# Kernel tuning notes

Measured on AMD Instinct MI355X. Metric: run time of the kernel, lower is better.

## Reference

```python
import jax, jax.numpy as jnp
import numpy as np

# ---- static config (mirrors GptOssDecoderLayer init) ----
H = 1024      # hidden_size
HD = 64       # head_size
NQ = 16       # num_query_heads
NKV = 4       # num_key_value_heads
G = NQ // NKV # num_key_value_groups
E = 8         # num_experts
TOPK = 2      # experts_per_token
FFN = 1024    # expert intermediate (== hidden in GPT-OSS)
B, Q = 4, 128 # batch sequences, new query tokens per sequence
P, PS = 8, 128
S = P * PS    # kv length per sequence
T = B * Q     # total query tokens
SW = 128      # sliding window (layer_idx % 2 == 0 -> active)
LIMIT = 7.0   # swiglu_limit
ALPHA = 1.702
EPS = 1e-5
NEG = -1e30
SCALE = HD ** -0.5


def rmsnorm(x, w):
    return x * w * jax.lax.rsqrt(jnp.mean(x * x, axis=-1, keepdims=True) + EPS)


def setup_inputs() -> dict:
    key = jax.random.key(0)
    ks = jax.random.split(key, 16)
    hidden = jax.random.normal(ks[0], (T, H), jnp.float32)
    kv_cache = jax.random.normal(ks[1], (B * P, 2, PS, NKV, HD), jnp.float32)
    kv_page_indices = jnp.arange(B * P, dtype=jnp.int32).reshape(B, P)
    # additive causal mask: query q sits at absolute position S - Q + q
    qpos = S - Q + jnp.arange(Q)
    kpos = jnp.arange(S)
    causal = qpos[:, None] >= kpos[None, :]
    attention_mask = jnp.broadcast_to(
        jnp.where(causal, 0.0, NEG).astype(jnp.float32), (B, Q, S))
    sinks = 0.1 * jax.random.normal(ks[2], (NQ,), jnp.float32)
    w_qkv = jax.random.normal(ks[3], (H, HD * (NQ + 2 * NKV)), jnp.float32) / np.sqrt(H)
    b_qkv = jnp.zeros((HD * (NQ + 2 * NKV),), jnp.float32)
    w_o = jax.random.normal(ks[4], (NQ * HD, H), jnp.float32) / np.sqrt(NQ * HD)
    b_o = jnp.zeros((H,), jnp.float32)
    ln1_w = jnp.ones((H,), jnp.float32)
    ln2_w = jnp.ones((H,), jnp.float32)
    w_router = jax.random.normal(ks[5], (H, E), jnp.float32) / np.sqrt(H)
    b_router = jnp.zeros((E,), jnp.float32)
    w_gate_up = jax.random.normal(ks[6], (E, H, 2 * FFN), jnp.float32) / np.sqrt(H)
    b_gate_up = jnp.zeros((E, 2 * FFN), jnp.float32)
    w_down = jax.random.normal(ks[7], (E, FFN, H), jnp.float32) / np.sqrt(FFN)
    b_down = jnp.zeros((E, H), jnp.float32)
    return dict(hidden=hidden, kv_cache=kv_cache, attention_mask=attention_mask,
                kv_page_indices=kv_page_indices, sinks=sinks, w_qkv=w_qkv,
                b_qkv=b_qkv, w_o=w_o, b_o=b_o, ln1_w=ln1_w, ln2_w=ln2_w,
                w_router=w_router, b_router=b_router, w_gate_up=w_gate_up,
                b_gate_up=b_gate_up, w_down=w_down, b_down=b_down)


def reference(hidden, kv_cache, attention_mask, kv_page_indices, sinks,
              w_qkv, b_qkv, w_o, b_o, ln1_w, ln2_w, w_router, b_router,
              w_gate_up, b_gate_up, w_down, b_down):
    # ---- attention block ----
    x = rmsnorm(hidden, ln1_w)
    qkv = x @ w_qkv + b_qkv                       # [T, HD*(NQ+2*NKV)]
    q = qkv[:, :NQ * HD].reshape(B, Q, NQ, HD)
    k_new = qkv[:, NQ * HD:(NQ + NKV) * HD].reshape(B, Q, NKV, HD)
    v_new = qkv[:, (NQ + NKV) * HD:].reshape(B, Q, NKV, HD)
    # gather paged KV cache -> [B, S, NKV, HD]; write new tokens into tail slots
    pages = kv_cache[kv_page_indices]             # [B, P, 2, PS, NKV, HD]
    K = pages[:, :, 0].reshape(B, S, NKV, HD).at[:, S - Q:].set(k_new)
    V = pages[:, :, 1].reshape(B, S, NKV, HD).at[:, S - Q:].set(v_new)
    Kr = jnp.repeat(K, G, axis=2)                 # GQA expand -> [B, S, NQ, HD]
    Vr = jnp.repeat(V, G, axis=2)
    scores = jnp.einsum('bqhd,bshd->bhqs', q * SCALE, Kr) + attention_mask[:, None]
    # sliding-window (module trims pages outside the window; equivalent mask)
    qpos = S - Q + jnp.arange(Q)
    kpos = jnp.arange(S)
    win_ok = (qpos[:, None] - kpos[None, :]) < SW
    scores = jnp.where(win_ok[None, None], scores, NEG)
    m = jnp.max(scores, axis=-1)
    m = jnp.where(jnp.isinf(m) & (m < 0), 0.0, m)
    p = jnp.exp(scores - m[..., None])            # [B, NQ, Q, S]
    # attention sink joins the softmax denominator (online-softmax correction)
    denom = jnp.sum(p, axis=-1) + jnp.exp(sinks[None, :, None] - m)
    attn = jnp.einsum('bhqs,bshd->bhqd', p, Vr) / denom[..., None]
    attn = attn.transpose(0, 2, 1, 3).reshape(T, NQ * HD)
    h = hidden + attn @ w_o + b_o
    # ---- MoE block ----
    x2 = rmsnorm(h, ln2_w)
    logits = x2 @ w_router + b_router             # [T, E]
    vals, idx = jax.lax.top_k(logits, TOPK)
    wts = jax.nn.softmax(vals, axis=-1)
    comb = jnp.sum(jax.nn.one_hot(idx, E, dtype=x2.dtype) * wts[..., None], axis=1)
    gu = jnp.einsum('th,ehf->etf', x2, w_gate_up) + b_gate_up[:, None, :]
    gate = jnp.minimum(gu[..., 0::2], LIMIT)
    up = jnp.clip(gu[..., 1::2], -LIMIT, LIMIT)
    glu = gate * jax.nn.sigmoid(gate * ALPHA)
    eo = jnp.einsum('etf,efh->eth', (up + 1.0) * glu, w_down) + b_down[:, None, :]
    moe = jnp.einsum('te,eth->th', comb, eo)
    return h + moe
```

## Files before the change

### kernel.cpp

```cpp
#include <hip/hip_runtime.h>

constexpr int H    = 1024;
constexpr int HD   = 64;
constexpr int NQ   = 16;
constexpr int NKV  = 4;
constexpr int E_   = 8;
constexpr int FFN  = 1024;
constexpr int B_   = 4;
constexpr int Q_   = 128;
constexpr int P_   = 8;
constexpr int PS   = 128;
constexpr int S_   = P_ * PS;
constexpr int T_   = B_ * Q_;
constexpr int QKV_N = HD * (NQ + 2 * NKV);
constexpr float EPS   = 1e-5f;
constexpr float ALPHA = 1.702f;
constexpr float LIMIT = 7.0f;
constexpr float SCALE = 0.125f;

constexpr int MAXROWS = 1536;
constexpr int MAXTILES = 24;

typedef __attribute__((ext_vector_type(4))) float f32x4;
typedef __attribute__((ext_vector_type(8))) short s16x8;

__device__ __forceinline__ unsigned short f2bf(float f) {
    unsigned u = __float_as_uint(f);
    u += 0x7FFFu + ((u >> 16) & 1u);
    return (unsigned short)(u >> 16);
}

__device__ __forceinline__ void lds_barrier() {
    asm volatile("s_waitcnt lgkmcnt(0)" ::: "memory");
    __builtin_amdgcn_s_barrier();
}

__global__ __launch_bounds__(256) void rmsnorm_kernel(const float* __restrict__ in,
                                                      const float* __restrict__ w,
                                                      unsigned short* __restrict__ outb,
                                                      int* __restrict__ cnt) {
    int t   = blockIdx.x;
    int tid = threadIdx.x;
    if (t == 0 && tid < E_) cnt[tid] = 0;
    float4 v = ((const float4*)(in + (size_t)t * H))[tid];
    float ss = v.x * v.x + v.y * v.y + v.z * v.z + v.w * v.w;
#pragma unroll
    for (int off = 32; off; off >>= 1) ss += __shfl_down(ss, off);
    __shared__ float partial[4];
    __shared__ float s_inv;
    if ((tid & 63) == 0) partial[tid >> 6] = ss;
    __syncthreads();
    if (tid == 0)
        s_inv = rsqrtf((partial[0] + partial[1] + partial[2] + partial[3]) * (1.0f / H) + EPS);
    __syncthreads();
    float inv = s_inv;
    float4 wv = ((const float4*)w)[tid];
    ushort4 ob;
    ob.x = f2bf(v.x * wv.x * inv); ob.y = f2bf(v.y * wv.y * inv);
    ob.z = f2bf(v.z * wv.z * inv); ob.w = f2bf(v.w * wv.w * inv);
    ((ushort4*)(outb + (size_t)t * H))[tid] = ob;
}

__global__ __launch_bounds__(256) void gemm_dense_t(const unsigned short* __restrict__ Abf,
                                                    const float* __restrict__ W,
                                                    const float* __restrict__ bias,
                                                    const float* __restrict__ resid,
                                                    float* __restrict__ C,
                                                    float* __restrict__ Cdup, int N) {
    int nb = blockIdx.x, mb = blockIdx.y * 64;
    int tid = threadIdx.x;
    int w = tid >> 6, lane = tid & 63;
    int r16 = lane & 15, kq = lane >> 4;
    int skb = tid >> 5, sn = tid & 31;

    __shared__ unsigned short WtA[8][32][8];
    __shared__ unsigned short WtB[8][32][8];

    size_t sN = (size_t)N;
    const float* wsrc = W + (size_t)(skb * 8) * sN + nb * 32 + sn;
    const unsigned short* ap = Abf + (size_t)(mb + w * 16 + r16) * 1024 + kq * 8;

    float wrA[8], wrB[8];
    s16x8 afA0, afA1, afB0, afB1;
    f32x4 acc0 = {}, acc1 = {};

#pragma unroll
    for (int j = 0; j < 8; j++) wrA[j] = wsrc[(size_t)j * sN];
    {
        s16x8 p;
#pragma unroll
        for (int j = 0; j < 8; j++) p[j] = (short)f2bf(wrA[j]);
        *(s16x8*)&WtA[skb][sn][0] = p;
    }
#pragma unroll
    for (int j = 0; j < 8; j++) wrA[j] = wsrc[(size_t)(64 + j) * sN];
    afA0 = *(const s16x8*)(ap);
    afA1 = *(const s16x8*)(ap + 32);
    lds_barrier();

    for (int s = 0; s < 8; s++) {
        int t0 = 2 * s;
        s16x8 b00 = *(const s16x8*)&WtA[kq][r16][0];
        s16x8 b01 = *(const s16x8*)&WtA[kq][16 + r16][0];
        s16x8 b10 = *(const s16x8*)&WtA[4 + kq][r16][0];
        s16x8 b11 = *(const s16x8*)&WtA[4 + kq][16 + r16][0];
        afB0 = *(const s16x8*)(ap + (t0 + 1) * 64);
        afB1 = *(const s16x8*)(ap + (t0 + 1) * 64 + 32);
        if (s < 7) {
#pragma unroll
            for (int j = 0; j < 8; j++) wrB[j] = wsrc[(size_t)((t0 + 2) * 64 + j) * sN];
        }
        acc0 = __builtin_amdgcn_mfma_f32_16x16x32_bf16(afA0, b00, acc0, 0, 0, 0);
        acc1 = __builtin_amdgcn_mfma_f32_16x16x32_bf16(afA0, b01, acc1, 0, 0, 0);
        acc0 = __builtin_amdgcn_mfma_f32_16x16x32_bf16(afA1, b10, acc0, 0, 0, 0);
        acc1 = __builtin_amdgcn_mfma_f32_16x16x32_bf16(afA1, b11, acc1, 0, 0, 0);
        {
            s16x8 p;
#pragma unroll
            for (int j = 0; j < 8; j++) p[j] = (short)f2bf(wrA[j]);
            *(s16x8*)&WtB[skb][sn][0] = p;
        }
        lds_barrier();
        s16x8 c00 = *(const s16x8*)&WtB[kq][r16][0];
        s16x8 c01 = *(const s16x8*)&WtB[kq][16 + r16][0];
        s16x8 c10 = *(const s16x8*)&WtB[4 + kq][r16][0];
        s16x8 c11 = *(const s16x8*)&WtB[4 + kq][16 + r16][0];
        if (s < 7) {
            afA0 = *(const s16x8*)(ap + (t0 + 2) * 64);
            afA1 = *(const s16x8*)(ap + (t0 + 2) * 64 + 32);
#pragma unroll
            for (int j = 0; j < 8; j++) wrA[j] = wsrc[(size_t)((t0 + 3) * 64 + j) * sN];
        }
        acc0 = __builtin_amdgcn_mfma_f32_16x16x32_bf16(afB0, c00, acc0, 0, 0, 0);
        acc1 = __builtin_amdgcn_mfma_f32_16x16x32_bf16(afB0, c01, acc1, 0, 0, 0);
        acc0 = __builtin_amdgcn_mfma_f32_16x16x32_bf16(afB1, c10, acc0, 0, 0, 0);
        acc1 = __builtin_amdgcn_mfma_f32_16x16x32_bf16(afB1, c11, acc1, 0, 0, 0);
        if (s < 7) {
            s16x8 p;
#pragma unroll
            for (int j = 0; j < 8; j++) p[j] = (short)f2bf(wrB[j]);
            *(s16x8*)&WtA[skb][sn][0] = p;
        }
        lds_barrier();
    }

    int row0 = mb + w * 16 + kq * 4;
    f32x4 accs[2] = {acc0, acc1};
#pragma unroll
    for (int nf = 0; nf < 2; nf++) {
        int col = nb * 32 + nf * 16 + r16;
        float bcol = bias[col];
#pragma unroll
        for (int r = 0; r < 4; r++) {
            int row = row0 + r;
            float v = accs[nf][r] + bcol;
            if (resid) v += resid[(size_t)row * sN + col];
            C[(size_t)row * sN + col] = v;
            if (Cdup) Cdup[(size_t)row * sN + col] = v;
        }
    }
}

__global__ __launch_bounds__(256) void attn_group_kernel(const float* __restrict__ qkv,
                                                         const float* __restrict__ kv_cache,
                                                         const int* __restrict__ page_idx,
                                                         const float* __restrict__ sinks,
                                                         unsigned short* __restrict__ attn_bf) {
    int blk = blockIdx.x;
    int kvh = blk & 3;
    int q   = (blk >> 2) & 127;
    int b   = blk >> 9;
    int t   = b * Q_ + q;
    int tid = threadIdx.x;
    int s_lo = S_ - Q_ - 127 + q;

    __shared__ __align__(16) float Vs[128][64];
    __shared__ __align__(16) float qs4[4][64];
    __shared__ float pv[4][128];
    __shared__ float sD[4];

#pragma unroll
    for (int r = 0; r < 8; r++) {
        int l = r * 256 + tid;
        int key = l >> 4, c = l & 15;
        int s = s_lo + key;
        const float* vp;
        if (s < S_ - Q_) {
            int page = page_idx[b * P_ + (s >> 7)];
            vp = kv_cache + (size_t)page * 65536 + 32768 + (size_t)(s & 127) * (NKV * HD) + kvh * HD;
        } else {
            vp = qkv + (size_t)(b * Q_ + (s - (S_ - Q_))) * QKV_N + (NQ + NKV) * HD + kvh * HD;
        }
        ((float4*)Vs[key])[c] = *(const float4*)(vp + c * 4);
    }
    {
        int hh = tid >> 6, d2 = tid & 63;
        qs4[hh][d2] = qkv[(size_t)t * QKV_N + (kvh * 4 + hh) * HD + d2];
    }
    __syncthreads();

    {
        int key = tid & 127, hp = tid >> 7;
        int s = s_lo + key;
        const float* kp;
        if (s < S_ - Q_) {
            int page = page_idx[b * P_ + (s >> 7)];
            kp = kv_cache + (size_t)page * 65536 + (size_t)(s & 127) * (NKV * HD) + kvh * HD;
        } else {
            kp = qkv + (size_t)(b * Q_ + (s - (S_ - Q_))) * QKV_N + NQ * HD + kvh * HD;
        }
        const float4* kp4 = (const float4*)kp;
        const float4* q0p = (const float4*)qs4[hp * 2];
        const float4* q1p = (const float4*)qs4[hp * 2 + 1];
        float sc0 = 0.f, sc1 = 0.f;
#pragma unroll
        for (int d4 = 0; d4 < 16; d4++) {
            float4 kk = kp4[d4];
            float4 q0 = q0p[d4], q1 = q1p[d4];
            sc0 += q0.x * kk.x + q0.y * kk.y + q0.z * kk.z + q0.w * kk.w;
            sc1 += q1.x * kk.x + q1.y * kk.y + q1.z * kk.z + q1.w * kk.w;
        }
        pv[hp * 2][key]     = sc0 * SCALE;
        pv[hp * 2 + 1][key] = sc1 * SCALE;
    }
    __syncthreads();

    {
        int wv = tid >> 6, lane = tid & 63;
        float a0 = pv[wv][lane], a1 = pv[wv][lane + 64];
        float m = fmaxf(a0, a1);
#pragma unroll
        for (int off = 32; off; off >>= 1) m = fmaxf(m, __shfl_xor(m, off));
        float p0 = __expf(a0 - m), p1 = __expf(a1 - m);
        float l = p0 + p1;
#pragma unroll
        for (int off = 32; off; off >>= 1) l += __shfl_xor(l, off);
        pv[wv][lane] = p0;
        pv[wv][lane + 64] = p1;
        if (lane == 0) sD[wv] = l + __expf(sinks[kvh * 4 + wv] - m);
    }
    __syncthreads();

    {
        int hh = tid >> 6, d2 = tid & 63;
        float a0 = 0.f, a1 = 0.f, a2 = 0.f, a3 = 0.f;
#pragma unroll 4
        for (int i = 0; i < 128; i += 4) {
            a0 += pv[hh][i]     * Vs[i][d2];
            a1 += pv[hh][i + 1] * Vs[i + 1][d2];
            a2 += pv[hh][i + 2] * Vs[i + 2][d2];
            a3 += pv[hh][i + 3] * Vs[i + 3][d2];
        }
        float acc = ((a0 + a1) + (a2 + a3)) / sD[hh];
        attn_bf[(size_t)t * (NQ * HD) + (kvh * 4 + hh) * HD + d2] = f2bf(acc);
    }
}

__global__ __launch_bounds__(256) void rms_router_kernel(const float* __restrict__ hbuf,
                                                         const float* __restrict__ ln2w,
                                                         const float* __restrict__ w_router,
                                                         const float* __restrict__ b_router,
                                                         unsigned short* __restrict__ x2bf,
                                                         int* __restrict__ ridx,
                                                         float* __restrict__ rwt,
                                                         int* __restrict__ cnt) {
    int t = blockIdx.x;
    int tid = threadIdx.x;
    float4 v = ((const float4*)(hbuf + (size_t)t * H))[tid];
    float ss = v.x * v.x + v.y * v.y + v.z * v.z + v.w * v.w;
#pragma unroll
    for (int off = 32; off; off >>= 1) ss += __shfl_down(ss, off);
    __shared__ float partial[4];
    __shared__ float s_inv;
    if ((tid & 63) == 0) partial[tid >> 6] = ss;
    __syncthreads();
    if (tid == 0)
        s_inv = rsqrtf((partial[0] + partial[1] + partial[2] + partial[3]) * (1.0f / H) + EPS);
    __syncthreads();
    float inv = s_inv;
    float4 wv = ((const float4*)ln2w)[tid];
    float4 o;
    o.x = v.x * wv.x * inv; o.y = v.y * wv.y * inv;
    o.z = v.z * wv.z * inv; o.w = v.w * wv.w * inv;
    ushort4 ob;
    ob.x = f2bf(o.x); ob.y = f2bf(o.y); ob.z = f2bf(o.z); ob.w = f2bf(o.w);
    ((ushort4*)(x2bf + (size_t)t * H))[tid] = ob;

    const float4* wr = (const float4*)(w_router + (size_t)tid * 4 * E_);
    float p[E_];
    {
        float4 r0a = wr[0], r0b = wr[1];
        float4 r1a = wr[2], r1b = wr[3];
        float4 r2a = wr[4], r2b = wr[5];
        float4 r3a = wr[6], r3b = wr[7];
        p[0] = o.x * r0a.x + o.y * r1a.x + o.z * r2a.x + o.w * r3a.x;
        p[1] = o.x * r0a.y + o.y * r1a.y + o.z * r2a.y + o.w * r3a.y;
        p[2] = o.x * r0a.z + o.y * r1a.z + o.z * r2a.z + o.w * r3a.z;
        p[3] = o.x * r0a.w + o.y * r1a.w + o.z * r2a.w + o.w * r3a.w;
        p[4] = o.x * r0b.x + o.y * r1b.x + o.z * r2b.x + o.w * r3b.x;
        p[5] = o.x * r0b.y + o.y * r1b.y + o.z * r2b.y + o.w * r3b.y;
        p[6] = o.x * r0b.z + o.y * r1b.z + o.z * r2b.z + o.w * r3b.z;
        p[7] = o.x * r0b.w + o.y * r1b.w + o.z * r2b.w + o.w * r3b.w;
    }
    __shared__ float wsum[4][E_];
    int wv2 = tid >> 6, lane = tid & 63;
#pragma unroll
    for (int e = 0; e < E_; e++) {
        float r = p[e];
#pragma unroll
        for (int off = 32; off; off >>= 1) r += __shfl_xor(r, off);
        if (lane == 0) wsum[wv2][e] = r;
    }
    __syncthreads();
    __shared__ float logits[E_];
    if (tid < E_)
        logits[tid] = wsum[0][tid] + wsum[1][tid] + wsum[2][tid] + wsum[3][tid] + b_router[tid];
    __syncthreads();
    if (tid == 0) {
        int i0 = 0; float v0 = logits[0];
        for (int ee = 1; ee < E_; ee++)
            if (logits[ee] > v0) { v0 = logits[ee]; i0 = ee; }
        int i1 = -1; float v1 = -3.4e38f;
        for (int ee = 0; ee < E_; ee++)
            if (ee != i0 && logits[ee] > v1) { v1 = logits[ee]; i1 = ee; }
        float w0 = 1.0f / (1.0f + __expf(v1 - v0));
        ridx[t * 2] = i0; ridx[t * 2 + 1] = i1;
        rwt[t * 2] = w0;  rwt[t * 2 + 1] = 1.0f - w0;
        atomicAdd(&cnt[i0], 1);
        atomicAdd(&cnt[i1], 1);
    }
}

__global__ __launch_bounds__(256) void plumb_kernel(const int* __restrict__ cnt,
                                                    const int* __restrict__ ridx,
                                                    int* __restrict__ poff,
                                                    int* __restrict__ list,
                                                    int* __restrict__ tmap) {
    __shared__ int lpos[E_], lpoff[E_];
    int tid = threadIdx.x;
    if (tid == 0) {
        int run = 0, it = 0;
        for (int e = 0; e < E_; e++) {
            lpoff[e] = run; poff[e] = run;
            int pc = (cnt[e] + 63) & ~63;
            for (int tl = 0; tl < (pc >> 6); tl++) tmap[1 + it++] = (e << 5) | tl;
            run += pc;
        }
        tmap[0] = it;
    }
    if (tid < E_) lpos[tid] = 0;
    __syncthreads();
    for (int i = tid; i < 2 * T_; i += 256) {
        int e = ridx[i];
        int pp = atomicAdd(&lpos[e], 1);
        list[lpoff[e] + pp] = i;
    }
}

__global__ __launch_bounds__(256) void moe_gateup_t(const unsigned short* __restrict__ x2bf,
                                                    const int* __restrict__ list,
                                                    const int* __restrict__ cnt,
                                                    const int* __restrict__ poff,
                                                    const int* __restrict__ tmap,
                                                    const float* __restrict__ wgu,
                                                    const float* __restrict__ bgu,
                                                    unsigned short* __restrict__ act_bf) {
    if ((int)blockIdx.y >= tmap[0]) return;
    int v0m = tmap[1 + blockIdx.y];
    int e = v0m >> 5, tl = v0m & 31;
    int n = cnt[e];
    int base = poff[e];
    int nb = blockIdx.x;
    int tid = threadIdx.x;
    int w = tid >> 6, lane = tid & 63;
    int r16 = lane & 15, kq = lane >> 4;
    int skb = tid >> 5, sn = tid & 31;

    __shared__ unsigned short WtA[8][32][8];
    __shared__ unsigned short WtB[8][32][8];

    const float* wsrc = wgu + (size_t)e * (1024 * 2048) + (size_t)(skb * 8) * 2048 + nb * 32 + sn;
    int rr0 = tl * 64 + w * 16 + r16;
    int t2a = (rr0 < n) ? list[base + rr0] : list[base];
    const unsigned short* ap = x2bf + (size_t)(t2a >> 1) * 1024 + kq * 8;

    float wrA[8], wrB[8];
    s16x8 afA0, afA1, afB0, afB1;
    f32x4 acc0 = {}, acc1 = {};

#pragma unroll
    for (int j = 0; j < 8; j++) wrA[j] = wsrc[(size_t)j * 2048];
    {
        s16x8 p;
#pragma unroll
        for (int j = 0; j < 8; j++) p[j] = (short)f2bf(wrA[j]);
        *(s16x8*)&WtA[skb][sn][0] = p;
    }
#pragma unroll
    for (int j = 0; j < 8; j++) wrA[j] = wsrc[(size_t)(64 + j) * 2048];
    afA0 = *(const s16x8*)(ap);
    afA1 = *(const s16x8*)(ap + 32);
    lds_barrier();

    for (int s = 0; s < 8; s++) {
        int t0 = 2 * s;
        s16x8 b00 = *(const s16x8*)&WtA[kq][r16][0];
        s16x8 b01 = *(const s16x8*)&WtA[kq][16 + r16][0];
        s16x8 b10 = *(const s16x8*)&WtA[4 + kq][r16][0];
        s16x8 b11 = *(const s16x8*)&WtA[4 + kq][16 + r16][0];
        afB0 = *(const s16x8*)(ap + (t0 + 1) * 64);
        afB1 = *(const s16x8*)(ap + (t0 + 1) * 64 + 32);
        if (s < 7) {
#pragma unroll
            for (int j = 0; j < 8; j++) wrB[j] = wsrc[(size_t)((t0 + 2) * 64 + j) * 2048];
        }
        acc0 = __builtin_amdgcn_mfma_f32_16x16x32_bf16(afA0, b00, acc0, 0, 0, 0);
        acc1 = __builtin_amdgcn_mfma_f32_16x16x32_bf16(afA0, b01, acc1, 0, 0, 0);
        acc0 = __builtin_amdgcn_mfma_f32_16x16x32_bf16(afA1, b10, acc0, 0, 0, 0);
        acc1 = __builtin_amdgcn_mfma_f32_16x16x32_bf16(afA1, b11, acc1, 0, 0, 0);
        {
            s16x8 p;
#pragma unroll
            for (int j = 0; j < 8; j++) p[j] = (short)f2bf(wrA[j]);
            *(s16x8*)&WtB[skb][sn][0] = p;
        }
        lds_barrier();
        s16x8 c00 = *(const s16x8*)&WtB[kq][r16][0];
        s16x8 c01 = *(const s16x8*)&WtB[kq][16 + r16][0];
        s16x8 c10 = *(const s16x8*)&WtB[4 + kq][r16][0];
        s16x8 c11 = *(const s16x8*)&WtB[4 + kq][16 + r16][0];
        if (s < 7) {
            afA0 = *(const s16x8*)(ap + (t0 + 2) * 64);
            afA1 = *(const s16x8*)(ap + (t0 + 2) * 64 + 32);
#pragma unroll
            for (int j = 0; j < 8; j++) wrA[j] = wsrc[(size_t)((t0 + 3) * 64 + j) * 2048];
        }
        acc0 = __builtin_amdgcn_mfma_f32_16x16x32_bf16(afB0, c00, acc0, 0, 0, 0);
        acc1 = __builtin_amdgcn_mfma_f32_16x16x32_bf16(afB0, c01, acc1, 0, 0, 0);
        acc0 = __builtin_amdgcn_mfma_f32_16x16x32_bf16(afB1, c10, acc0, 0, 0, 0);
        acc1 = __builtin_amdgcn_mfma_f32_16x16x32_bf16(afB1, c11, acc1, 0, 0, 0);
        if (s < 7) {
            s16x8 p;
#pragma unroll
            for (int j = 0; j < 8; j++) p[j] = (short)f2bf(wrB[j]);
            *(s16x8*)&WtA[skb][sn][0] = p;
        }
        lds_barrier();
    }

    int parity = r16 & 1;
    f32x4 accs[2] = {acc0, acc1};
#pragma unroll
    for (int nf = 0; nf < 2; nf++) {
        int gucol = nb * 32 + nf * 16 + r16;
        float bb = bgu[(size_t)e * 2048 + gucol];
#pragma unroll
        for (int r = 0; r < 4; r++) {
            float v = accs[nf][r] + bb;
            float o = __shfl_xor(v, 1);
            if (!parity) {
                float g = fminf(v, LIMIT);
                float u = fminf(fmaxf(o, -LIMIT), LIMIT);
                float glu = g / (1.0f + __expf(-ALPHA * g));
                int rr = tl * 64 + w * 16 + kq * 4 + r;
                if (rr < n)
                    act_bf[(size_t)(base + rr) * FFN + (gucol >> 1)] = f2bf((u + 1.0f) * glu);
            }
        }
    }
}

__global__ __launch_bounds__(256) void moe_down_t(const unsigned short* __restrict__ act_bf,
                                                  const int* __restrict__ list,
                                                  const int* __restrict__ cnt,
                                                  const int* __restrict__ poff,
                                                  const int* __restrict__ tmap,
                                                  const float* __restrict__ rwt,
                                                  const float* __restrict__ wdn,
                                                  const float* __restrict__ b_down,
                                                  float* __restrict__ out) {
    if ((int)blockIdx.y >= tmap[0]) return;
    int v0m = tmap[1 + blockIdx.y];
    int e = v0m >> 5, tl = v0m & 31;
    int n = cnt[e];
    int base = poff[e];
    int nb = blockIdx.x;
    int z  = blockIdx.z;
    int tid = threadIdx.x;
    int w = tid >> 6, lane = tid & 63;
    int r16 = lane & 15, kq = lane >> 4;
    int skb = tid >> 5, sn = tid & 31;

    __shared__ unsigned short WtA[8][32][8];
    __shared__ unsigned short WtB[8][32][8];

    const float* wsrc = wdn + (size_t)e * (1024 * 1024) + (size_t)(z * 512 + skb * 8) * 1024 + nb * 32 + sn;
    const unsigned short* ap = act_bf + (size_t)(base + tl * 64 + w * 16 + r16) * 1024 + z * 512 + kq * 8;

    float wrA[8], wrB[8];
    s16x8 afA0, afA1, afB0, afB1;
    f32x4 acc0 = {}, acc1 = {};

#pragma unroll
    for (int j = 0; j < 8; j++) wrA[j] = wsrc[(size_t)j * 1024];
    {
        s16x8 p;
#pragma unroll
        for (int j = 0; j < 8; j++) p[j] = (short)f2bf(wrA[j]);
        *(s16x8*)&WtA[skb][sn][0] = p;
    }
#pragma unroll
    for (int j = 0; j < 8; j++) wrA[j] = wsrc[(size_t)(64 + j) * 1024];
    afA0 = *(const s16x8*)(ap);
    afA1 = *(const s16x8*)(ap + 32);
    lds_barrier();

    for (int s = 0; s < 4; s++) {
        int t0 = 2 * s;
        s16x8 b00 = *(const s16x8*)&WtA[kq][r16][0];
        s16x8 b01 = *(const s16x8*)&WtA[kq][16 + r16][0];
        s16x8 b10 = *(const s16x8*)&WtA[4 + kq][r16][0];
        s16x8 b11 = *(const s16x8*)&WtA[4 + kq][16 + r16][0];
        afB0 = *(const s16x8*)(ap + (t0 + 1) * 64);
        afB1 = *(const s16x8*)(ap + (t0 + 1) * 64 + 32);
        if (s < 3) {
#pragma unroll
            for (int j = 0; j < 8; j++) wrB[j] = wsrc[(size_t)((t0 + 2) * 64 + j) * 1024];
        }
        acc0 = __builtin_amdgcn_mfma_f32_16x16x32_bf16(afA0, b00, acc0, 0, 0, 0);
        acc1 = __builtin_amdgcn_mfma_f32_16x16x32_bf16(afA0, b01, acc1, 0, 0, 0);
        acc0 = __builtin_amdgcn_mfma_f32_16x16x32_bf16(afA1, b10, acc0, 0, 0, 0);
        acc1 = __builtin_amdgcn_mfma_f32_16x16x32_bf16(afA1, b11, acc1, 0, 0, 0);
        {
            s16x8 p;
#pragma unroll
            for (int j = 0; j < 8; j++) p[j] = (short)f2bf(wrA[j]);
            *(s16x8*)&WtB[skb][sn][0] = p;
        }
        lds_barrier();
        s16x8 c00 = *(const s16x8*)&WtB[kq][r16][0];
        s16x8 c01 = *(const s16x8*)&WtB[kq][16 + r16][0];
        s16x8 c10 = *(const s16x8*)&WtB[4 + kq][r16][0];
        s16x8 c11 = *(const s16x8*)&WtB[4 + kq][16 + r16][0];
        if (s < 3) {
            afA0 = *(const s16x8*)(ap + (t0 + 2) * 64);
            afA1 = *(const s16x8*)(ap + (t0 + 2) * 64 + 32);
#pragma unroll
            for (int j = 0; j < 8; j++) wrA[j] = wsrc[(size_t)((t0 + 3) * 64 + j) * 1024];
        }
        acc0 = __builtin_amdgcn_mfma_f32_16x16x32_bf16(afB0, c00, acc0, 0, 0, 0);
        acc1 = __builtin_amdgcn_mfma_f32_16x16x32_bf16(afB0, c01, acc1, 0, 0, 0);
        acc0 = __builtin_amdgcn_mfma_f32_16x16x32_bf16(afB1, c10, acc0, 0, 0, 0);
        acc1 = __builtin_amdgcn_mfma_f32_16x16x32_bf16(afB1, c11, acc1, 0, 0, 0);
        if (s < 3) {
            s16x8 p;
#pragma unroll
            for (int j = 0; j < 8; j++) p[j] = (short)f2bf(wrB[j]);
            *(s16x8*)&WtA[skb][sn][0] = p;
        }
        lds_barrier();
    }

    f32x4 accs[2] = {acc0, acc1};
#pragma unroll
    for (int r = 0; r < 4; r++) {
        int rr = tl * 64 + w * 16 + kq * 4 + r;
        if (rr < n) {
            int t2 = list[base + rr];
            float sc = rwt[t2];
            float* op = out + (size_t)(t2 >> 1) * H;
#pragma unroll
            for (int nf = 0; nf < 2; nf++) {
                int col = nb * 32 + nf * 16 + r16;
                float v = accs[nf][r] + (z == 0 ? b_down[(size_t)e * 1024 + col] : 0.0f);
                atomicAdd(op + col, sc * v);
            }
        }
    }
}

extern "C" void kernel_launch(void* const* d_in, const int* in_sizes, int n_in,
                              void* d_out, int out_size, void* d_ws, size_t ws_size,
                              hipStream_t stream) {
    const float* hidden          = (const float*)d_in[0];
    const float* kv_cache        = (const float*)d_in[1];
    const int*   kv_page_indices = (const int*)d_in[3];
    const float* sinks           = (const float*)d_in[4];
    const float* w_qkv           = (const float*)d_in[5];
    const float* b_qkv           = (const float*)d_in[6];
    const float* w_o             = (const float*)d_in[7];
    const float* b_o             = (const float*)d_in[8];
    const float* ln1_w           = (const float*)d_in[9];
    const float* ln2_w           = (const float*)d_in[10];
    const float* w_router        = (const float*)d_in[11];
    const float* b_router        = (const float*)d_in[12];
    const float* w_gate_up       = (const float*)d_in[13];
    const float* b_gate_up       = (const float*)d_in[14];
    const float* w_down          = (const float*)d_in[15];
    const float* b_down          = (const float*)d_in[16];
    float* out = (float*)d_out;

    char* base = (char*)d_ws;
    float* qkv   = (float*)base;                       base += (size_t)T_ * QKV_N * 4;
    float* hbuf  = (float*)base;                       base += (size_t)T_ * H * 4;
    unsigned short* x_bf    = (unsigned short*)base;   base += (size_t)T_ * H * 2;
    unsigned short* x2_bf   = (unsigned short*)base;   base += (size_t)T_ * H * 2;
    unsigned short* attn_bf = (unsigned short*)base;   base += (size_t)T_ * NQ * HD * 2;
    unsigned short* act_bf  = (unsigned short*)base;   base += (size_t)(MAXROWS + 128) * FFN * 2;
    float* rwt  = (float*)base;                        base += 2 * T_ * 4;
    int*   ridx = (int*)base;                          base += 2 * T_ * 4;
    int*   cnt  = (int*)base;                          base += E_ * 4;
    int*   poff = (int*)base;                          base += E_ * 4;
    int*   list = (int*)base;                          base += MAXROWS * 4;
    int*   tmap = (int*)base;                          base += (1 + MAXTILES + 7) * 4;

    rmsnorm_kernel<<<T_, 256, 0, stream>>>(hidden, ln1_w, x_bf, cnt);
    gemm_dense_t<<<dim3(QKV_N / 32, T_ / 64), 256, 0, stream>>>(
        x_bf, w_qkv, b_qkv, nullptr, qkv, nullptr, QKV_N);
    attn_group_kernel<<<B_ * Q_ * NKV, 256, 0, stream>>>(qkv, kv_cache, kv_page_indices, sinks, attn_bf);
    gemm_dense_t<<<dim3(H / 32, T_ / 64), 256, 0, stream>>>(
        attn_bf, w_o, b_o, hidden, hbuf, out, H);
    rms_router_kernel<<<T_, 256, 0, stream>>>(hbuf, ln2_w, w_router, b_router,
                                              x2_bf, ridx, rwt, cnt);
    plumb_kernel<<<1, 256, 0, stream>>>(cnt, ridx, poff, list, tmap);
    moe_gateup_t<<<dim3(FFN * 2 / 32, MAXTILES), 256, 0, stream>>>(
        x2_bf, list, cnt, poff, tmap, w_gate_up, b_gate_up, act_bf);
    moe_down_t<<<dim3(H / 32, MAXTILES, 2), 256, 0, stream>>>(
        act_bf, list, cnt, poff, tmap, rwt, w_down, b_down, out);
}
```

Measured before the change: 275.3 us.

## Split-K the dense GEMMs in two with atomic accumulation and pre-initialized outputs

Adds an init kernel that pre-fills the qkv buffer with its bias and hbuf/out with hidden plus the output bias. Both dense GEMMs are then launched with a z dimension of 2, each half covering 512 of the K range, and their partial sums are accumulated with float atomicAdd. This doubles the block count to fill more compute units for these small-N GEMMs. In exchange it costs an extra launch, memory traffic for the init pass, atomic write contention, and run-to-run nondeterministic summation order.

```diff
diff --git a/kernel.cpp b/kernel.cpp
--- a/kernel.cpp
+++ b/kernel.cpp
@@ -35,6 +35,30 @@
     __builtin_amdgcn_s_barrier();
 }
 
+__global__ __launch_bounds__(256) void init_outputs(const float* __restrict__ hidden,
+                                                    const float* __restrict__ b_qkv,
+                                                    const float* __restrict__ b_o,
+                                                    float* __restrict__ qkv,
+                                                    float* __restrict__ hbuf,
+                                                    float* __restrict__ out) {
+    int i = blockIdx.x * 256 + threadIdx.x;
+    constexpr int NQKV4 = T_ * QKV_N / 4;
+    constexpr int NH4   = T_ * H / 4;
+    if (i < NQKV4) {
+        ((float4*)qkv)[i] = ((const float4*)b_qkv)[i % (QKV_N / 4)];
+    } else {
+        int j = i - NQKV4;
+        if (j < NH4) {
+            float4 h = ((const float4*)hidden)[j];
+            float4 b = ((const float4*)b_o)[j % (H / 4)];
+            float4 v;
+            v.x = h.x + b.x; v.y = h.y + b.y; v.z = h.z + b.z; v.w = h.w + b.w;
+            ((float4*)hbuf)[j] = v;
+            ((float4*)out)[j] = v;
+        }
+    }
+}
+
 __global__ __launch_bounds__(256) void rmsnorm_kernel(const float* __restrict__ in,
                                                       const float* __restrict__ w,
                                                       unsigned short* __restrict__ outb,
@@ -63,11 +87,10 @@
 
 __global__ __launch_bounds__(256) void gemm_dense_t(const unsigned short* __restrict__ Abf,
                                                     const float* __restrict__ W,
-                                                    const float* __restrict__ bias,
-                                                    const float* __restrict__ resid,
                                                     float* __restrict__ C,
                                                     float* __restrict__ Cdup, int N) {
     int nb = blockIdx.x, mb = blockIdx.y * 64;
+    int z  = blockIdx.z;
     int tid = threadIdx.x;
     int w = tid >> 6, lane = tid & 63;
     int r16 = lane & 15, kq = lane >> 4;
@@ -77,8 +100,8 @@
     __shared__ unsigned short WtB[8][32][8];
 
     size_t sN = (size_t)N;
-    const float* wsrc = W + (size_t)(skb * 8) * sN + nb * 32 + sn;
-    const unsigned short* ap = Abf + (size_t)(mb + w * 16 + r16) * 1024 + kq * 8;
+    const float* wsrc = W + (size_t)(z * 512 + skb * 8) * sN + nb * 32 + sn;
+    const unsigned short* ap = Abf + (size_t)(mb + w * 16 + r16) * 1024 + z * 512 + kq * 8;
 
     float wrA[8], wrB[8];
     s16x8 afA0, afA1, afB0, afB1;
@@ -98,7 +121,7 @@
     afA1 = *(const s16x8*)(ap + 32);
     lds_barrier();
 
-    for (int s = 0; s < 8; s++) {
+    for (int s = 0; s < 4; s++) {
         int t0 = 2 * s;
         s16x8 b00 = *(const s16x8*)&WtA[kq][r16][0];
         s16x8 b01 = *(const s16x8*)&WtA[kq][16 + r16][0];
@@ -106,7 +129,7 @@
         s16x8 b11 = *(const s16x8*)&WtA[4 + kq][16 + r16][0];
         afB0 = *(const s16x8*)(ap + (t0 + 1) * 64);
         afB1 = *(const s16x8*)(ap + (t0 + 1) * 64 + 32);
-        if (s < 7) {
+        if (s < 3) {
 #pragma unroll
             for (int j = 0; j < 8; j++) wrB[j] = wsrc[(size_t)((t0 + 2) * 64 + j) * sN];
         }
@@ -125,7 +148,7 @@
         s16x8 c01 = *(const s16x8*)&WtB[kq][16 + r16][0];
         s16x8 c10 = *(const s16x8*)&WtB[4 + kq][r16][0];
         s16x8 c11 = *(const s16x8*)&WtB[4 + kq][16 + r16][0];
-        if (s < 7) {
+        if (s < 3) {
             afA0 = *(const s16x8*)(ap + (t0 + 2) * 64);
             afA1 = *(const s16x8*)(ap + (t0 + 2) * 64 + 32);
 #pragma unroll
@@ -135,7 +158,7 @@
         acc1 = __builtin_amdgcn_mfma_f32_16x16x32_bf16(afB0, c01, acc1, 0, 0, 0);
         acc0 = __builtin_amdgcn_mfma_f32_16x16x32_bf16(afB1, c10, acc0, 0, 0, 0);
         acc1 = __builtin_amdgcn_mfma_f32_16x16x32_bf16(afB1, c11, acc1, 0, 0, 0);
-        if (s < 7) {
+        if (s < 3) {
             s16x8 p;
 #pragma unroll
             for (int j = 0; j < 8; j++) p[j] = (short)f2bf(wrB[j]);
@@ -149,14 +172,11 @@
 #pragma unroll
     for (int nf = 0; nf < 2; nf++) {
         int col = nb * 32 + nf * 16 + r16;
-        float bcol = bias[col];
 #pragma unroll
         for (int r = 0; r < 4; r++) {
             int row = row0 + r;
-            float v = accs[nf][r] + bcol;
-            if (resid) v += resid[(size_t)row * sN + col];
-            C[(size_t)row * sN + col] = v;
-            if (Cdup) Cdup[(size_t)row * sN + col] = v;
+            atomicAdd(&C[(size_t)row * sN + col], accs[nf][r]);
+            if (Cdup) atomicAdd(&Cdup[(size_t)row * sN + col], accs[nf][r]);
         }
     }
 }
@@ -614,12 +634,14 @@
     int*   list = (int*)base;                          base += MAXROWS * 4;
     int*   tmap = (int*)base;                          base += (1 + MAXTILES + 7) * 4;
 
+    init_outputs<<<(T_ * QKV_N / 4 + T_ * H / 4 + 255) / 256, 256, 0, stream>>>(
+        hidden, b_qkv, b_o, qkv, hbuf, out);
     rmsnorm_kernel<<<T_, 256, 0, stream>>>(hidden, ln1_w, x_bf, cnt);
-    gemm_dense_t<<<dim3(QKV_N / 32, T_ / 64), 256, 0, stream>>>(
-        x_bf, w_qkv, b_qkv, nullptr, qkv, nullptr, QKV_N);
+    gemm_dense_t<<<dim3(QKV_N / 32, T_ / 64, 2), 256, 0, stream>>>(
+        x_bf, w_qkv, qkv, nullptr, QKV_N);
     attn_group_kernel<<<B_ * Q_ * NKV, 256, 0, stream>>>(qkv, kv_cache, kv_page_indices, sinks, attn_bf);
-    gemm_dense_t<<<dim3(H / 32, T_ / 64), 256, 0, stream>>>(
-        attn_bf, w_o, b_o, hidden, hbuf, out, H);
+    gemm_dense_t<<<dim3(H / 32, T_ / 64, 2), 256, 0, stream>>>(
+        attn_bf, w_o, hbuf, out, H);
     rms_router_kernel<<<T_, 256, 0, stream>>>(hbuf, ln2_w, w_router, b_router,
                                               x2_bf, ridx, rwt, cnt);
     plumb_kernel<<<1, 256, 0, stream>>>(cnt, ridx, poff, list, tmap);
```

Result: slower. 281.7 us (+2.3%).

## Split-K the MoE gate-up GEMM and move SwiGLU into a separate reduction kernel

Applied to the files above, without the earlier changes.

Splits the gate-up expert GEMM along K into two halves on a third grid dimension, doubling the block count. Each half writes raw fp32 partial sums to a new workspace buffer. A new swiglu kernel sums the two partials, adds the bias, applies the clamped SwiGLU and writes bf16 activations. The aim is better GPU occupancy on the weight-bandwidth-bound GEMM, at the cost of an extra launch and extra fp32 global traffic for the partials.

```diff
diff --git a/kernel.cpp b/kernel.cpp
--- a/kernel.cpp
+++ b/kernel.cpp
@@ -357,20 +357,20 @@
     }
 }
 
-__global__ __launch_bounds__(256) void moe_gateup_t(const unsigned short* __restrict__ x2bf,
-                                                    const int* __restrict__ list,
-                                                    const int* __restrict__ cnt,
-                                                    const int* __restrict__ poff,
-                                                    const int* __restrict__ tmap,
-                                                    const float* __restrict__ wgu,
-                                                    const float* __restrict__ bgu,
-                                                    unsigned short* __restrict__ act_bf) {
+__global__ __launch_bounds__(256) void moe_gateup_sk(const unsigned short* __restrict__ x2bf,
+                                                     const int* __restrict__ list,
+                                                     const int* __restrict__ cnt,
+                                                     const int* __restrict__ poff,
+                                                     const int* __restrict__ tmap,
+                                                     const float* __restrict__ wgu,
+                                                     float* __restrict__ gupart) {
     if ((int)blockIdx.y >= tmap[0]) return;
     int v0m = tmap[1 + blockIdx.y];
     int e = v0m >> 5, tl = v0m & 31;
     int n = cnt[e];
     int base = poff[e];
     int nb = blockIdx.x;
+    int z  = blockIdx.z;
     int tid = threadIdx.x;
     int w = tid >> 6, lane = tid & 63;
     int r16 = lane & 15, kq = lane >> 4;
@@ -379,10 +379,10 @@
     __shared__ unsigned short WtA[8][32][8];
     __shared__ unsigned short WtB[8][32][8];
 
-    const float* wsrc = wgu + (size_t)e * (1024 * 2048) + (size_t)(skb * 8) * 2048 + nb * 32 + sn;
+    const float* wsrc = wgu + (size_t)e * (1024 * 2048) + (size_t)(z * 512 + skb * 8) * 2048 + nb * 32 + sn;
     int rr0 = tl * 64 + w * 16 + r16;
     int t2a = (rr0 < n) ? list[base + rr0] : list[base];
-    const unsigned short* ap = x2bf + (size_t)(t2a >> 1) * 1024 + kq * 8;
+    const unsigned short* ap = x2bf + (size_t)(t2a >> 1) * 1024 + z * 512 + kq * 8;
 
     float wrA[8], wrB[8];
     s16x8 afA0, afA1, afB0, afB1;
@@ -402,7 +402,7 @@
     afA1 = *(const s16x8*)(ap + 32);
     lds_barrier();
 
-    for (int s = 0; s < 8; s++) {
+    for (int s = 0; s < 4; s++) {
         int t0 = 2 * s;
         s16x8 b00 = *(const s16x8*)&WtA[kq][r16][0];
         s16x8 b01 = *(const s16x8*)&WtA[kq][16 + r16][0];
@@ -410,7 +410,7 @@
         s16x8 b11 = *(const s16x8*)&WtA[4 + kq][16 + r16][0];
         afB0 = *(const s16x8*)(ap + (t0 + 1) * 64);
         afB1 = *(const s16x8*)(ap + (t0 + 1) * 64 + 32);
-        if (s < 7) {
+        if (s < 3) {
 #pragma unroll
             for (int j = 0; j < 8; j++) wrB[j] = wsrc[(size_t)((t0 + 2) * 64 + j) * 2048];
         }
@@ -429,7 +429,7 @@
         s16x8 c01 = *(const s16x8*)&WtB[kq][16 + r16][0];
         s16x8 c10 = *(const s16x8*)&WtB[4 + kq][r16][0];
         s16x8 c11 = *(const s16x8*)&WtB[4 + kq][16 + r16][0];
-        if (s < 7) {
+        if (s < 3) {
             afA0 = *(const s16x8*)(ap + (t0 + 2) * 64);
             afA1 = *(const s16x8*)(ap + (t0 + 2) * 64 + 32);
 #pragma unroll
@@ -439,7 +439,7 @@
         acc1 = __builtin_amdgcn_mfma_f32_16x16x32_bf16(afB0, c01, acc1, 0, 0, 0);
         acc0 = __builtin_amdgcn_mfma_f32_16x16x32_bf16(afB1, c10, acc0, 0, 0, 0);
         acc1 = __builtin_amdgcn_mfma_f32_16x16x32_bf16(afB1, c11, acc1, 0, 0, 0);
-        if (s < 7) {
+        if (s < 3) {
             s16x8 p;
 #pragma unroll
             for (int j = 0; j < 8; j++) p[j] = (short)f2bf(wrB[j]);
@@ -448,25 +448,45 @@
         lds_barrier();
     }
 
-    int parity = r16 & 1;
+    float* gp = gupart + (size_t)z * MAXROWS * 2048;
     f32x4 accs[2] = {acc0, acc1};
 #pragma unroll
     for (int nf = 0; nf < 2; nf++) {
         int gucol = nb * 32 + nf * 16 + r16;
-        float bb = bgu[(size_t)e * 2048 + gucol];
 #pragma unroll
         for (int r = 0; r < 4; r++) {
-            float v = accs[nf][r] + bb;
-            float o = __shfl_xor(v, 1);
-            if (!parity) {
-                float g = fminf(v, LIMIT);
-                float u = fminf(fmaxf(o, -LIMIT), LIMIT);
-                float glu = g / (1.0f + __expf(-ALPHA * g));
-                int rr = tl * 64 + w * 16 + kq * 4 + r;
-                if (rr < n)
-                    act_bf[(size_t)(base + rr) * FFN + (gucol >> 1)] = f2bf((u + 1.0f) * glu);
-            }
-        }
+            int rr = tl * 64 + w * 16 + kq * 4 + r;
+            gp[(size_t)(base + rr) * 2048 + gucol] = accs[nf][r];
+        }
+    }
+}
+
+__global__ __launch_bounds__(256) void swiglu_kernel(const float* __restrict__ gupart,
+                                                     const int* __restrict__ cnt,
+                                                     const int* __restrict__ poff,
+                                                     const int* __restrict__ tmap,
+                                                     const float* __restrict__ bgu,
+                                                     unsigned short* __restrict__ act_bf) {
+    if ((int)blockIdx.y >= tmap[0]) return;
+    int v0m = tmap[1 + blockIdx.y];
+    int e = v0m >> 5, tl = v0m & 31;
+    int n = cnt[e];
+    int base = poff[e];
+    int tid = threadIdx.x;
+    int fc = blockIdx.x * 256 + tid;
+    float2 b2 = *(const float2*)(bgu + (size_t)e * 2048 + 2 * fc);
+    const float* p0 = gupart + (size_t)(base + tl * 64) * 2048 + 2 * fc;
+    const float* p1 = p0 + (size_t)MAXROWS * 2048;
+    int rmax = n - tl * 64; if (rmax > 64) rmax = 64;
+    for (int r = 0; r < rmax; r++) {
+        float2 v0 = *(const float2*)(p0 + (size_t)r * 2048);
+        float2 v1 = *(const float2*)(p1 + (size_t)r * 2048);
+        float g = v0.x + v1.x + b2.x;
+        float u = v0.y + v1.y + b2.y;
+        float gate = fminf(g, LIMIT);
+        float up = fminf(fmaxf(u, -LIMIT), LIMIT);
+        float glu = gate / (1.0f + __expf(-ALPHA * gate));
+        act_bf[(size_t)(base + tl * 64 + r) * FFN + fc] = f2bf((up + 1.0f) * glu);
     }
 }
 
@@ -607,6 +627,7 @@
     unsigned short* x2_bf   = (unsigned short*)base;   base += (size_t)T_ * H * 2;
     unsigned short* attn_bf = (unsigned short*)base;   base += (size_t)T_ * NQ * HD * 2;
     unsigned short* act_bf  = (unsigned short*)base;   base += (size_t)(MAXROWS + 128) * FFN * 2;
+    float* gupart = (float*)base;                      base += (size_t)2 * MAXROWS * 2048 * 4;
     float* rwt  = (float*)base;                        base += 2 * T_ * 4;
     int*   ridx = (int*)base;                          base += 2 * T_ * 4;
     int*   cnt  = (int*)base;                          base += E_ * 4;
@@ -623,8 +644,10 @@
     rms_router_kernel<<<T_, 256, 0, stream>>>(hbuf, ln2_w, w_router, b_router,
                                               x2_bf, ridx, rwt, cnt);
     plumb_kernel<<<1, 256, 0, stream>>>(cnt, ridx, poff, list, tmap);
-    moe_gateup_t<<<dim3(FFN * 2 / 32, MAXTILES), 256, 0, stream>>>(
-        x2_bf, list, cnt, poff, tmap, w_gate_up, b_gate_up, act_bf);
+    moe_gateup_sk<<<dim3(FFN * 2 / 32, MAXTILES, 2), 256, 0, stream>>>(
+        x2_bf, list, cnt, poff, tmap, w_gate_up, gupart);
+    swiglu_kernel<<<dim3(4, MAXTILES), 256, 0, stream>>>(
+        gupart, cnt, poff, tmap, b_gate_up, act_bf);
     moe_down_t<<<dim3(H / 32, MAXTILES, 2), 256, 0, stream>>>(
         act_bf, list, cnt, poff, tmap, rwt, w_down, b_down, out);
 }
```

Measured after the change: 297.2 us. 8.0% more time.
